# Kernel optimization log

Measured on AMD Instinct MI355X. Metric: run time of the kernel, lower is better.

Reference implementation:

```python
import jax, jax.numpy as jnp
import numpy as np

GRID_SIZE = 5
SPLINE_ORDER = 3
GRID_MIN, GRID_MAX = -1.0, 1.0
LN_EPS = 1e-5


def _make_grid():
    # Extended knot grid shared across input features: (grid_size + 2*order + 1,)
    h = (GRID_MAX - GRID_MIN) / GRID_SIZE
    return jnp.arange(-SPLINE_ORDER, GRID_SIZE + SPLINE_ORDER + 1, dtype=jnp.float32) * h + GRID_MIN


def b_splines(x, grid):
    # x: (B, in) -> bases: (B, in, grid_size + spline_order)
    xe = x[..., None]  # (B, in, 1)
    bases = ((xe >= grid[:-1]) & (xe < grid[1:])).astype(x.dtype)
    for k in range(1, SPLINE_ORDER + 1):
        left = (xe - grid[: -(k + 1)]) / (grid[k:-1] - grid[: -(k + 1)])
        right = (grid[k + 1:] - xe) / (grid[k + 1:] - grid[1:-k])
        bases = left * bases[..., :-1] + right * bases[..., 1:]
    return bases


def setup_inputs() -> dict:
    key = jax.random.key(0)
    ks = jax.random.split(key, 5)
    B, IN, OUT, COEF = 16384, 1024, 512, GRID_SIZE + SPLINE_ORDER
    return {
        "rgb_features": jax.random.normal(ks[0], (B, IN // 2), jnp.float32),
        "tactile_features": jax.random.normal(ks[1], (B, IN // 2), jnp.float32),
        "base_weight": jax.random.normal(ks[2], (OUT, IN), jnp.float32) * 0.02,
        "spline_weight": jax.random.normal(ks[3], (OUT, IN, COEF), jnp.float32) * 0.02,
        "spline_scaler": 1.0 + 0.02 * jax.random.normal(ks[4], (OUT, IN), jnp.float32),
        "ln_gamma": jnp.ones((OUT,), jnp.float32),
        "ln_beta": jnp.zeros((OUT,), jnp.float32),
    }


def reference(rgb_features, tactile_features, base_weight, spline_weight, spline_scaler, ln_gamma, ln_beta):
    x = jnp.concatenate((rgb_features, tactile_features), axis=1)  # (B, 1024)
    grid = _make_grid()
    # KANLinear: base path (SiLU + linear) + spline path (B-spline basis + linear)
    base_out = jnp.einsum("bi,oi->bo", jax.nn.silu(x), base_weight)
    bases = b_splines(x, grid)  # (B, in, coef)
    scaled_w = spline_weight * spline_scaler[..., None]  # (out, in, coef)
    spline_out = jnp.einsum("bik,oik->bo", bases, scaled_w)
    fused = base_out + spline_out
    # LayerNorm over last dim
    mu = jnp.mean(fused, axis=-1, keepdims=True)
    var = jnp.var(fused, axis=-1, keepdims=True)
    fused = (fused - mu) * jax.lax.rsqrt(var + LN_EPS) * ln_gamma + ln_beta
    # Dropout is identity in eval mode
    return fused
```

## Files before the change

kernel.cpp:

```cpp
#include <hip/hip_runtime.h>
#include <cstdint>
#include <cstddef>


#define BATCH    16384
#define OUT_DIM  512
#define KTOT     9216
#define BM       128
#define BK       64
#define NCHUNK        144
#define SPLINE_CHUNKS 128

typedef __attribute__((ext_vector_type(8))) short  short8;
typedef __attribute__((ext_vector_type(4))) float  f32x4;

static __device__ __forceinline__ unsigned short f2bf(float f) {
    unsigned int u = __float_as_uint(f);
    unsigned int r = u + 0x7fffu + ((u >> 16) & 1u);
    return (unsigned short)(r >> 16);
}

__global__ void prep_w_kernel(const float* __restrict__ bw,
                              const float* __restrict__ sw,
                              const float* __restrict__ sc,
                              unsigned short* __restrict__ Wp) {
    int t = blockIdx.x * 256 + threadIdx.x;
    int o = t / 1152;
    int g = t - o * 1152;
    int sz = o & 7;
    unsigned short o8[8];
    size_t dst;
    if (g < 1024) {
        float s = sc[(size_t)o * 1024 + g];
        const float* w = sw + ((size_t)o * 1024 + g) * 8;
        #pragma unroll
        for (int k = 0; k < 8; ++k) o8[k] = f2bf(w[k] * s);
        dst = (size_t)o * KTOT + (size_t)(g >> 3) * 64 + (size_t)(((g & 7) ^ sz)) * 8;
    } else {
        int gi = g - 1024;
        const float* w = bw + (size_t)o * 1024 + gi * 8;
        #pragma unroll
        for (int k = 0; k < 8; ++k) o8[k] = f2bf(w[k]);
        dst = (size_t)o * KTOT + (size_t)8192 + (size_t)(gi >> 3) * 64 + (size_t)(((gi & 7) ^ sz)) * 8;
    }
    *reinterpret_cast<short8*>(Wp + dst) = *reinterpret_cast<const short8*>(o8);
}

static __device__ __forceinline__ void basis8(float x, unsigned* out) {
    float tpos = (x + 2.2f) * 2.5f;
    float fj   = floorf(tpos);
    int   j    = (int)fj;
    float u  = tpos - fj;
    float v  = 1.f - u;
    float u2 = u * u;
    float u3 = u2 * u;
    const float c6 = 1.f / 6.f;
    float n0 = v * v * v * c6;
    float n1 = (3.f * u3 - 6.f * u2 + 4.f) * c6;
    float n2 = (-3.f * u3 + 3.f * u2 + 3.f * u + 1.f) * c6;
    float n3 = u3 * c6;
    unsigned p0, p1;
    asm("v_cvt_pk_bf16_f32 %0, %1, %2" : "=v"(p0) : "v"(n0), "v"(n1));
    asm("v_cvt_pk_bf16_f32 %0, %1, %2" : "=v"(p1) : "v"(n2), "v"(n3));
    int sh = (j << 4) - 48;
    int c  = sh & 16;
    int w  = (sh - c) >> 5;
    unsigned long long P = ((unsigned long long)p1 << 32) | p0;
    unsigned long long T = P << c;
    unsigned t0 = (unsigned)T;
    unsigned t1 = (unsigned)(T >> 32);
    unsigned t2 = c ? (p1 >> 16) : 0u;
    #pragma unroll
    for (int i = 0; i < 4; ++i) {
        unsigned r = 0u;
        r = (w == i    ) ? t0 : r;
        r = (w == i - 1) ? t1 : r;
        r = (w == i - 2) ? t2 : r;
        out[i] = r;
    }
}

template<bool SPLIT>
__launch_bounds__(1024, 4)
__global__ void kan_gemm_kernel(const float* __restrict__ rgb,
                                const float* __restrict__ tac,
                                const unsigned short* __restrict__ Wp,
                                float* __restrict__ dest_base) {
    __shared__ unsigned short At[BM][BK];
    __shared__ unsigned short Bt[2][OUT_DIM][BK];

    const int tid  = threadIdx.x;
    const int lane = tid & 63;
    const int wid  = tid >> 6;
    const int b0   = blockIdx.x * BM;
    const int wr   = wid & 1;
    const int wc   = wid >> 1;
    const int ksp  = SPLIT ? (int)blockIdx.y : 0;
    const int kc0  = SPLIT ? (ksp ? 72 : 0)             : 0;
    const int kcS  = SPLIT ? (ksp ? SPLINE_CHUNKS : 72) : SPLINE_CHUNKS;
    const int kc1  = SPLIT ? (ksp ? NCHUNK : 72)        : NCHUNK;
    float* dest = dest_base + (size_t)ksp * BATCH * OUT_DIM;

    const int ar = tid >> 3;
    const int af_ = tid & 7;

    f32x4 acc[4][4];
    #pragma unroll
    for (int m = 0; m < 4; ++m)
        #pragma unroll
        for (int n = 0; n < 4; ++n)
            acc[m][n] = (f32x4){0.f, 0.f, 0.f, 0.f};

    auto mfma_step = [&](int buf) {
        #pragma unroll
        for (int ks = 0; ks < 2; ++ks) {
            int cb = ks * 4 + (lane >> 4);
            short8 afr[4];
            #pragma unroll
            for (int m = 0; m < 4; ++m) {
                int row = wr * 64 + m * 16 + (lane & 15);
                afr[m] = *reinterpret_cast<const short8*>(&At[row][(cb ^ (row & 7)) * 8]);
            }
            #pragma unroll
            for (int n = 0; n < 4; ++n) {
                int row = wc * 64 + n * 16 + (lane & 15);
                short8 bfr = *reinterpret_cast<const short8*>(
                    &Bt[buf][row][(cb ^ (row & 7)) * 8]);
                #pragma unroll
                for (int m = 0; m < 4; ++m)
                    acc[m][n] = __builtin_amdgcn_mfma_f32_16x16x32_bf16(
                        afr[m], bfr, acc[m][n], 0, 0, 0);
            }
        }
    };

    auto loadx_s = [&](int c) -> float {
        int i0 = c * 8;
        const float* xs = (i0 < 512) ? rgb : tac;
        int ic = i0 & 511;
        return xs[(size_t)(b0 + ar) * 512 + ic + af_];
    };

    auto loadx_b = [&](int c, f32x4& xa, f32x4& xb) {
        int i0 = (c - SPLINE_CHUNKS) * 64;
        const float* xs = (i0 < 512) ? rgb : tac;
        int ic = i0 & 511;
        const float* xp = xs + (size_t)(b0 + ar) * 512 + ic + af_ * 8;
        xa = *reinterpret_cast<const f32x4*>(xp);
        xb = *reinterpret_cast<const f32x4*>(xp + 4);
    };

    auto silupack = [&](const f32x4& xa, const f32x4& xb, unsigned* o) {
        float s[8];
        #pragma unroll
        for (int q = 0; q < 4; ++q) {
            float a = xa[q]; s[q]     = a / (1.f + __expf(-a));
            float b = xb[q]; s[q + 4] = b / (1.f + __expf(-b));
        }
        #pragma unroll
        for (int q = 0; q < 4; ++q)
            asm("v_cvt_pk_bf16_f32 %0, %1, %2"
                : "=v"(o[q]) : "v"(s[2 * q]), "v"(s[2 * q + 1]));
    };

    auto writeA = [&](const unsigned* o4) {
        *reinterpret_cast<short8*>(&At[ar][(af_ ^ (ar & 7)) * 8]) =
            *reinterpret_cast<const short8*>(o4);
    };

    auto gload_B = [&](int kc, int buf) {
        int k0g = kc * BK;
        #pragma unroll
        for (int rp = 0; rp < 4; ++rp) {
            int row0 = wid * 32 + rp * 8;
            const unsigned short* gp =
                Wp + (size_t)(row0 + (lane >> 3)) * KTOT + k0g + (lane & 7) * 8;
            __builtin_amdgcn_global_load_lds(
                (const __attribute__((address_space(1))) unsigned int*)gp,
                (__attribute__((address_space(3))) unsigned int*)&Bt[buf][row0][0],
                16, 0, 0);
        }
    };

    {
        float x0 = loadx_s(kc0);
        gload_B(kc0, 0);
        unsigned o4[4];
        basis8(x0, o4);
        writeA(o4);
        asm volatile("s_waitcnt vmcnt(0) lgkmcnt(0)" ::: "memory");
        __builtin_amdgcn_s_barrier();
        asm volatile("" ::: "memory");
    }

    for (int t = kc0; t < kcS; ++t) {
        const int  buf   = (t - kc0) & 1;
        const bool moreB = (t + 1 < kc1);
        const bool moreA = (t + 1 < kcS);
        float xn = 0.f;
        if (moreA) xn = loadx_s(t + 1);
        asm volatile("" ::: "memory");
        if (moreB) gload_B(t + 1, buf ^ 1);
        mfma_step(buf);
        unsigned o4[4];
        if (moreA) basis8(xn, o4);
        __builtin_amdgcn_sched_barrier(0);
        __builtin_amdgcn_s_barrier();
        asm volatile("" ::: "memory");
        if (moreA) writeA(o4);
        asm volatile("s_waitcnt vmcnt(0) lgkmcnt(0)" ::: "memory");
        __builtin_amdgcn_sched_barrier(0);
        __builtin_amdgcn_s_barrier();
        asm volatile("" ::: "memory");
    }

    if (kcS < kc1) {
        {
            f32x4 xa, xb;
            loadx_b(kcS, xa, xb);
            unsigned o4[4];
            silupack(xa, xb, o4);
            writeA(o4);
            asm volatile("s_waitcnt vmcnt(0) lgkmcnt(0)" ::: "memory");
            __builtin_amdgcn_s_barrier();
            asm volatile("" ::: "memory");
        }
        for (int t = kcS; t < kc1; ++t) {
            const int  buf   = (t - kc0) & 1;
            const bool more  = (t + 1 < kc1);
            f32x4 xa, xb;
            if (more) loadx_b(t + 1, xa, xb);
            asm volatile("" ::: "memory");
            if (more) gload_B(t + 1, buf ^ 1);
            mfma_step(buf);
            unsigned o4[4];
            if (more) silupack(xa, xb, o4);
            __builtin_amdgcn_sched_barrier(0);
            __builtin_amdgcn_s_barrier();
            asm volatile("" ::: "memory");
            if (more) writeA(o4);
            asm volatile("s_waitcnt vmcnt(0) lgkmcnt(0)" ::: "memory");
            __builtin_amdgcn_sched_barrier(0);
            __builtin_amdgcn_s_barrier();
            asm volatile("" ::: "memory");
        }
    }

    #pragma unroll
    for (int m = 0; m < 4; ++m) {
        int row = b0 + wr * 64 + m * 16 + ((lane >> 4) << 2);
        #pragma unroll
        for (int n = 0; n < 4; ++n) {
            int col = wc * 64 + n * 16 + (lane & 15);
            #pragma unroll
            for (int jj = 0; jj < 4; ++jj)
                dest[(size_t)(row + jj) * OUT_DIM + col] = acc[m][n][jj];
        }
    }
}

__global__ void reduce_ln_kernel(const float* __restrict__ P0,
                                 const float* __restrict__ P1,
                                 const float* __restrict__ gamma,
                                 const float* __restrict__ beta,
                                 float* __restrict__ out) {
    int row  = blockIdx.x * 4 + (threadIdx.x >> 6);
    int lane = threadIdx.x & 63;
    const float* p0 = P0 + (size_t)row * OUT_DIM;
    const float* p1 = P1 + (size_t)row * OUT_DIM;
    f32x4 a0 = *reinterpret_cast<const f32x4*>(p0 + lane * 4);
    f32x4 a1 = *reinterpret_cast<const f32x4*>(p0 + 256 + lane * 4);
    f32x4 b0 = *reinterpret_cast<const f32x4*>(p1 + lane * 4);
    f32x4 b1 = *reinterpret_cast<const f32x4*>(p1 + 256 + lane * 4);
    f32x4 v0, v1;
    #pragma unroll
    for (int q = 0; q < 4; ++q) { v0[q] = a0[q] + b0[q]; v1[q] = a1[q] + b1[q]; }
    float s = 0.f, ss = 0.f;
    #pragma unroll
    for (int q = 0; q < 4; ++q) {
        s  += v0[q] + v1[q];
        ss += v0[q] * v0[q] + v1[q] * v1[q];
    }
    #pragma unroll
    for (int off = 1; off < 64; off <<= 1) {
        s  += __shfl_xor(s, off);
        ss += __shfl_xor(ss, off);
    }
    float mu  = s * (1.f / 512.f);
    float var = ss * (1.f / 512.f) - mu * mu;
    float rs  = rsqrtf(var + 1e-5f);
    f32x4 g0 = *reinterpret_cast<const f32x4*>(gamma + lane * 4);
    f32x4 g1 = *reinterpret_cast<const f32x4*>(gamma + 256 + lane * 4);
    f32x4 e0 = *reinterpret_cast<const f32x4*>(beta + lane * 4);
    f32x4 e1 = *reinterpret_cast<const f32x4*>(beta + 256 + lane * 4);
    float* po = out + (size_t)row * OUT_DIM;
    f32x4 r0, r1;
    #pragma unroll
    for (int q = 0; q < 4; ++q) {
        r0[q] = (v0[q] - mu) * rs * g0[q] + e0[q];
        r1[q] = (v1[q] - mu) * rs * g1[q] + e1[q];
    }
    *reinterpret_cast<f32x4*>(po + lane * 4)       = r0;
    *reinterpret_cast<f32x4*>(po + 256 + lane * 4) = r1;
}

__global__ void ln_kernel(float* __restrict__ io,
                          const float* __restrict__ gamma,
                          const float* __restrict__ beta) {
    int row  = blockIdx.x * 4 + (threadIdx.x >> 6);
    int lane = threadIdx.x & 63;
    float* p = io + (size_t)row * OUT_DIM;
    f32x4 v0 = *reinterpret_cast<const f32x4*>(p + lane * 4);
    f32x4 v1 = *reinterpret_cast<const f32x4*>(p + 256 + lane * 4);
    float s = 0.f, ss = 0.f;
    #pragma unroll
    for (int q = 0; q < 4; ++q) {
        s  += v0[q] + v1[q];
        ss += v0[q] * v0[q] + v1[q] * v1[q];
    }
    #pragma unroll
    for (int off = 1; off < 64; off <<= 1) {
        s  += __shfl_xor(s, off);
        ss += __shfl_xor(ss, off);
    }
    float mu  = s * (1.f / 512.f);
    float var = ss * (1.f / 512.f) - mu * mu;
    float rs  = rsqrtf(var + 1e-5f);
    f32x4 g0 = *reinterpret_cast<const f32x4*>(gamma + lane * 4);
    f32x4 g1 = *reinterpret_cast<const f32x4*>(gamma + 256 + lane * 4);
    f32x4 e0 = *reinterpret_cast<const f32x4*>(beta + lane * 4);
    f32x4 e1 = *reinterpret_cast<const f32x4*>(beta + 256 + lane * 4);
    f32x4 r0, r1;
    #pragma unroll
    for (int q = 0; q < 4; ++q) {
        r0[q] = (v0[q] - mu) * rs * g0[q] + e0[q];
        r1[q] = (v1[q] - mu) * rs * g1[q] + e1[q];
    }
    *reinterpret_cast<f32x4*>(p + lane * 4)       = r0;
    *reinterpret_cast<f32x4*>(p + 256 + lane * 4) = r1;
}

extern "C" void kernel_launch(void* const* d_in, const int* in_sizes, int n_in,
                              void* d_out, int out_size, void* d_ws, size_t ws_size,
                              hipStream_t stream) {
    const float* rgb   = (const float*)d_in[0];
    const float* tac   = (const float*)d_in[1];
    const float* bw    = (const float*)d_in[2];
    const float* sw    = (const float*)d_in[3];
    const float* sc    = (const float*)d_in[4];
    const float* gamma = (const float*)d_in[5];
    const float* beta  = (const float*)d_in[6];
    float* out = (float*)d_out;
    unsigned short* Wp = (unsigned short*)d_ws;

    prep_w_kernel<<<2304, 256, 0, stream>>>(bw, sw, sc, Wp);

    const size_t PART = (size_t)BATCH * OUT_DIM * sizeof(float);
    const size_t POFF = 16ull << 20;
    if (ws_size >= POFF + 2 * PART) {
        float* P = (float*)((char*)d_ws + POFF);
        dim3 g(BATCH / BM, 2);
        kan_gemm_kernel<true><<<g, 1024, 0, stream>>>(rgb, tac, Wp, P);
        reduce_ln_kernel<<<BATCH / 4, 256, 0, stream>>>(
            P, P + (size_t)BATCH * OUT_DIM, gamma, beta, out);
    } else {
        dim3 g(BATCH / BM, 1);
        kan_gemm_kernel<false><<<g, 1024, 0, stream>>>(rgb, tac, Wp, out);
        ln_kernel<<<BATCH / 4, 256, 0, stream>>>(out, gamma, beta);
    }
}
```

Baseline: 191.0 us.

## Double-buffer A tile and prefetch B two chunks ahead with partial vmcnt waits

Adds a second LDS buffer for the activation tile so the next chunk's basis/SiLU values are written before the current MFMA step. B weight tiles are now prefetched two chunks ahead and waited on with vmcnt(4) instead of vmcnt(0), keeping one load group in flight across the barrier. X loads are also prefetched two iterations ahead. This is meant to hide global-load latency behind MFMA work, at the cost of extra LDS (16 KB more) and more fragile waitcnt accounting.

```diff
diff --git a/kernel.cpp b/kernel.cpp
--- a/kernel.cpp
+++ b/kernel.cpp
@@ -86,7 +86,7 @@
                                 const float* __restrict__ tac,
                                 const unsigned short* __restrict__ Wp,
                                 float* __restrict__ dest_base) {
-    __shared__ unsigned short At[BM][BK];
+    __shared__ unsigned short At[2][BM][BK];
     __shared__ unsigned short Bt[2][OUT_DIM][BK];
 
     const int tid  = threadIdx.x;
@@ -101,7 +101,7 @@
     const int kc1  = SPLIT ? (ksp ? NCHUNK : 72)        : NCHUNK;
     float* dest = dest_base + (size_t)ksp * BATCH * OUT_DIM;
 
-    const int ar = tid >> 3;
+    const int ar  = tid >> 3;
     const int af_ = tid & 7;
 
     f32x4 acc[4][4];
@@ -111,7 +111,7 @@
         for (int n = 0; n < 4; ++n)
             acc[m][n] = (f32x4){0.f, 0.f, 0.f, 0.f};
 
-    auto mfma_step = [&](int buf) {
+    auto mfma_step = [&](int ab, int bb) {
         #pragma unroll
         for (int ks = 0; ks < 2; ++ks) {
             int cb = ks * 4 + (lane >> 4);
@@ -119,13 +119,13 @@
             #pragma unroll
             for (int m = 0; m < 4; ++m) {
                 int row = wr * 64 + m * 16 + (lane & 15);
-                afr[m] = *reinterpret_cast<const short8*>(&At[row][(cb ^ (row & 7)) * 8]);
+                afr[m] = *reinterpret_cast<const short8*>(&At[ab][row][(cb ^ (row & 7)) * 8]);
             }
             #pragma unroll
             for (int n = 0; n < 4; ++n) {
                 int row = wc * 64 + n * 16 + (lane & 15);
                 short8 bfr = *reinterpret_cast<const short8*>(
-                    &Bt[buf][row][(cb ^ (row & 7)) * 8]);
+                    &Bt[bb][row][(cb ^ (row & 7)) * 8]);
                 #pragma unroll
                 for (int m = 0; m < 4; ++m)
                     acc[m][n] = __builtin_amdgcn_mfma_f32_16x16x32_bf16(
@@ -163,8 +163,8 @@
                 : "=v"(o[q]) : "v"(s[2 * q]), "v"(s[2 * q + 1]));
     };
 
-    auto writeA = [&](const unsigned* o4) {
-        *reinterpret_cast<short8*>(&At[ar][(af_ ^ (ar & 7)) * 8]) =
+    auto writeA = [&](const unsigned* o4, int ab) {
+        *reinterpret_cast<short8*>(&At[ab][ar][(af_ ^ (ar & 7)) * 8]) =
             *reinterpret_cast<const short8*>(o4);
     };
 
@@ -182,67 +182,77 @@
         }
     };
 
+    gload_B(kc0, 0);
+    gload_B(kc0 + 1 < kc1 ? kc0 + 1 : kc1 - 1, 1);
     {
         float x0 = loadx_s(kc0);
-        gload_B(kc0, 0);
         unsigned o4[4];
         basis8(x0, o4);
-        writeA(o4);
-        asm volatile("s_waitcnt vmcnt(0) lgkmcnt(0)" ::: "memory");
-        __builtin_amdgcn_s_barrier();
-        asm volatile("" ::: "memory");
-    }
+        writeA(o4, 0);
+    }
+    float xn = (kc0 + 1 < kcS) ? loadx_s(kc0 + 1) : 0.f;
+    asm volatile("s_waitcnt vmcnt(4) lgkmcnt(0)" ::: "memory");
+    __builtin_amdgcn_sched_barrier(0);
+    __builtin_amdgcn_s_barrier();
+    __builtin_amdgcn_sched_barrier(0);
 
     for (int t = kc0; t < kcS; ++t) {
         const int  buf   = (t - kc0) & 1;
-        const bool moreB = (t + 1 < kc1);
         const bool moreA = (t + 1 < kcS);
-        float xn = 0.f;
-        if (moreA) xn = loadx_s(t + 1);
-        asm volatile("" ::: "memory");
-        if (moreB) gload_B(t + 1, buf ^ 1);
-        mfma_step(buf);
         unsigned o4[4];
-        if (moreA) basis8(xn, o4);
+        if (moreA) {
+            basis8(xn, o4);
+            writeA(o4, buf ^ 1);
+        }
+        if (t + 2 < kcS) xn = loadx_s(t + 2);
+        mfma_step(buf, buf);
         __builtin_amdgcn_sched_barrier(0);
         __builtin_amdgcn_s_barrier();
-        asm volatile("" ::: "memory");
-        if (moreA) writeA(o4);
-        asm volatile("s_waitcnt vmcnt(0) lgkmcnt(0)" ::: "memory");
+        __builtin_amdgcn_sched_barrier(0);
+        int tn = (t + 2 < kc1) ? t + 2 : kc1 - 1;
+        gload_B(tn, buf);
+        asm volatile("s_waitcnt vmcnt(4) lgkmcnt(0)" ::: "memory");
         __builtin_amdgcn_sched_barrier(0);
         __builtin_amdgcn_s_barrier();
-        asm volatile("" ::: "memory");
+        __builtin_amdgcn_sched_barrier(0);
     }
 
     if (kcS < kc1) {
+        f32x4 xa{}, xb{};
         {
-            f32x4 xa, xb;
-            loadx_b(kcS, xa, xb);
+            f32x4 a0, b0;
+            loadx_b(kcS, a0, b0);
             unsigned o4[4];
-            silupack(xa, xb, o4);
-            writeA(o4);
-            asm volatile("s_waitcnt vmcnt(0) lgkmcnt(0)" ::: "memory");
+            silupack(a0, b0, o4);
+            writeA(o4, (kcS - kc0) & 1);
+            if (kcS + 1 < kc1) loadx_b(kcS + 1, xa, xb);
+            asm volatile("s_waitcnt lgkmcnt(0)" ::: "memory");
+            __builtin_amdgcn_sched_barrier(0);
             __builtin_amdgcn_s_barrier();
-            asm volatile("" ::: "memory");
+            __builtin_amdgcn_sched_barrier(0);
         }
         for (int t = kcS; t < kc1; ++t) {
             const int  buf   = (t - kc0) & 1;
-            const bool more  = (t + 1 < kc1);
-            f32x4 xa, xb;
-            if (more) loadx_b(t + 1, xa, xb);
-            asm volatile("" ::: "memory");
-            if (more) gload_B(t + 1, buf ^ 1);
-            mfma_step(buf);
+            const bool moreA = (t + 1 < kc1);
             unsigned o4[4];
-            if (more) silupack(xa, xb, o4);
+            if (moreA) {
+                silupack(xa, xb, o4);
+                writeA(o4, buf ^ 1);
+            }
+            f32x4 na, nb;
+            const bool moreX = (t + 2 < kc1);
+            if (moreX) loadx_b(t + 2, na, nb);
+            mfma_step(buf, buf);
             __builtin_amdgcn_sched_barrier(0);
             __builtin_amdgcn_s_barrier();
-            asm volatile("" ::: "memory");
-            if (more) writeA(o4);
-            asm volatile("s_waitcnt vmcnt(0) lgkmcnt(0)" ::: "memory");
+            __builtin_amdgcn_sched_barrier(0);
+            int tn = moreX ? t + 2 : kc1 - 1;
+            gload_B(tn, buf);
+            asm volatile("s_waitcnt vmcnt(4) lgkmcnt(0)" ::: "memory");
             __builtin_amdgcn_sched_barrier(0);
             __builtin_amdgcn_s_barrier();
-            asm volatile("" ::: "memory");
+            __builtin_amdgcn_sched_barrier(0);
+            if (moreX) { xa = na; xb = nb; }
         }
     }
 
```

New measurement: 184.2 us, median of 2. -3.5%, faster.
